# Optimization experiments

Measured on AMD Instinct MI355X. Metric: run time of the kernel, lower is better.

## Reference

```python
import jax, jax.numpy as jnp
import numpy as np

B, P = 8, 1000          # batch_size, num_prots
N = B * P               # total PPI nodes
E = 512000              # edges (avg degree 64)
F_HPO = 1024            # HPO feature dim (num_features)
F_MOLP = 8192           # protein molecular feature dim (hardcoded)
F_MOLD = 1024           # drug molecular feature dim (hardcoded)
D = 200
EPS = 1e-8              # torch CosineSimilarity default eps


def leaky(x):
    return jax.nn.leaky_relu(x, 0.2)


def gcn_improved(x, W, b, src, dst):
    # PyG GCNConv(improved=True): A_hat = A + 2*I, symmetrically normalized.
    h = x @ W                                                   # [N,200]
    deg = jnp.zeros((x.shape[0],), x.dtype).at[dst].add(1.0) + 2.0
    dinv = jax.lax.rsqrt(deg)
    norm = dinv[src] * dinv[dst]                                # [E]
    out = jnp.zeros_like(h).at[dst].add(norm[:, None] * h[src])  # gather->scale->scatter
    out = out + (2.0 * dinv * dinv)[:, None] * h                # self loops with weight 2
    return out + b


def setup_inputs() -> dict:
    key = jax.random.key(0)
    ks = jax.random.split(key, 30)
    def W(i, shape):
        return jax.random.normal(ks[i], shape, jnp.float32) * (1.0 / float(np.sqrt(shape[0])))
    def bvec(i, n):
        return jax.random.normal(ks[i], (n,), jnp.float32) * 0.01
    return {
        # forward inputs
        'PPI_x': jax.random.normal(ks[0], (N, F_HPO), jnp.float32),
        'protein_mol_feature': jax.random.normal(ks[1], (N, F_MOLP), jnp.float32),
        'drug_feature': jax.random.normal(ks[2], (B, F_HPO), jnp.float32),
        'drug_mol_feature': jax.random.normal(ks[3], (B, F_MOLD), jnp.float32),
        'edge_index': jax.random.randint(ks[4], (2, E), 0, N, dtype=jnp.int32),
        # frozen HPO model heads (assumed Linear -> 200)
        'hpo_drug_W': W(5, (F_HPO, D)), 'hpo_drug_b': bvec(6, D),
        'hpo_prot_W': W(7, (F_HPO, D)), 'hpo_prot_b': bvec(8, D),
        # mol_protein_model: 8192 -> 256 -> 200
        'mp_W1': W(9, (F_MOLP, 256)), 'mp_b1': bvec(10, 256),
        'mp_W2': W(11, (256, D)), 'mp_b2': bvec(12, D),
        # mol_drug_model: 1024 -> 256 -> 200
        'md_W1': W(13, (F_MOLD, 256)), 'md_b1': bvec(14, 256),
        'md_W2': W(15, (256, D)), 'md_b2': bvec(16, D),
        # fusion linears
        'pl1_W': W(17, (2 * D, D)), 'pl1_b': bvec(18, D),
        'dl1_W': W(19, (2 * D, D)), 'dl1_b': bvec(20, D),
        'dl2_W': W(21, (D, D)), 'dl2_b': bvec(22, D),
        # GCN layers
        'g1_W': W(23, (D, D)), 'g1_b': bvec(24, D),
        'g2_W': W(25, (D, D)), 'g2_b': bvec(26, D),
    }


def reference(PPI_x, protein_mol_feature, drug_feature, drug_mol_feature, edge_index,
              hpo_drug_W, hpo_drug_b, hpo_prot_W, hpo_prot_b,
              mp_W1, mp_b1, mp_W2, mp_b2, md_W1, md_b1, md_W2, md_b2,
              pl1_W, pl1_b, dl1_W, dl1_b, dl2_W, dl2_b,
              g1_W, g1_b, g2_W, g2_b):
    src, dst = edge_index[0], edge_index[1]
    # protein branch (dropout is identity in eval)
    px = PPI_x @ hpo_prot_W + hpo_prot_b                                 # [N,200]
    pm = leaky(protein_mol_feature @ mp_W1 + mp_b1) @ mp_W2 + mp_b2      # [N,200]
    px = leaky(jnp.concatenate([px, pm], axis=1))                        # [N,400]
    px = px @ pl1_W + pl1_b                                              # [N,200]
    # drug branch
    df = drug_feature @ hpo_drug_W + hpo_drug_b                          # [B,200]
    dm = leaky(drug_mol_feature @ md_W1 + md_b1) @ md_W2 + md_b2         # [B,200]
    d = leaky(jnp.concatenate([dm, df], axis=1))                         # [B,400]
    d = leaky(d @ dl1_W + dl1_b)                                         # [B,200]
    d = d @ dl2_W + dl2_b                                                # [B,200]
    d = jnp.repeat(d, P, axis=0)                                         # [B*P,200]
    # two stacked GCN layers (no nonlinearity between, as in source)
    px = gcn_improved(px, g1_W, g1_b, src, dst)
    px = gcn_improved(px, g2_W, g2_b, src, dst)
    # per-row cosine similarity (torch.nn.CosineSimilarity(dim=1))
    num = jnp.sum(d * px, axis=1)
    den = jnp.maximum(jnp.linalg.norm(d, axis=1), EPS) * jnp.maximum(jnp.linalg.norm(px, axis=1), EPS)
    sim = num / den
    return jax.nn.sigmoid(sim.reshape(B, P))
```

## Files before the change

### kernel.cpp

```cpp
#include <hip/hip_runtime.h>
#include <cstdint>
#include <cstddef>

typedef uint16_t u16;
typedef __bf16 bf16x8 __attribute__((ext_vector_type(8)));
typedef short  s16x8  __attribute__((ext_vector_type(8)));
typedef float  f32x4  __attribute__((ext_vector_type(4)));

__device__ __forceinline__ u16 f2b(float f) {
    union { float f; uint32_t u; } v; v.f = f;
    uint32_t u = v.u;
    uint32_t r = (u + 0x7FFFu + ((u >> 16) & 1u)) >> 16;
    return (u16)r;
}
__device__ __forceinline__ float b2f(u16 h) {
    union { uint32_t u; float f; } v; v.u = ((uint32_t)h) << 16;
    return v.f;
}
__device__ __forceinline__ float leakyf(float x) { return x > 0.f ? x : 0.2f * x; }
__device__ __forceinline__ void unp4(uint2 u, float& f0, float& f1, float& f2, float& f3) {
    union { uint32_t u; float f; } t;
    t.u = u.x << 16;          f0 = t.f;
    t.u = u.x & 0xffff0000u;  f1 = t.f;
    t.u = u.y << 16;          f2 = t.f;
    t.u = u.y & 0xffff0000u;  f3 = t.f;
}

static constexpr int NN = 8000;
static constexpr int EE = 512000;
static constexpr int BB = 8;

#define GLOAD_LDS16(gp, lp)                                                              \
    __builtin_amdgcn_global_load_lds((const __attribute__((address_space(1))) void*)(gp), \
                                     (__attribute__((address_space(3))) void*)(lp), 16, 0, 0)

__global__ void conv_wT(const float* __restrict__ W, int Wn, int rows, int rowOff,
                        u16* __restrict__ Bt, int Kpad, int kOff, int kSpan) {
    __shared__ u16 tile[64][65];
    const int kb = blockIdx.x * 64, nb = blockIdx.y * 64;
    const int tid = threadIdx.x;
    const int ln = tid & 63, lw = tid >> 6;
    #pragma unroll
    for (int r = 0; r < 16; r++) {
        int kk = kb + lw * 16 + r;
        int n  = nb + ln;
        float v = (kk < rows && n < Wn) ? W[(size_t)(rowOff + kk) * Wn + n] : 0.f;
        tile[ln][lw * 16 + r] = f2b(v);
    }
    __syncthreads();
    #pragma unroll
    for (int r = 0; r < 16; r++) {
        int nl = lw * 16 + r;
        int kk = kb + ln;
        if (kk < kSpan) Bt[(size_t)(nb + nl) * Kpad + kOff + kk] = tile[nl][ln];
    }
}

__global__ void conv_wT5(const float* W_mp2, const float* W_pl1, const float* W_g1, const float* W_g2,
                         u16* Btmp2, u16* Btpl1, u16* Btg1, u16* Btg2) {
    __shared__ u16 tile[64][65];
    const float* W; int Wn, rows, rowOff; u16* Bt; int Kpad, kOff, kSpan;
    switch (blockIdx.z) {
        case 0: W = W_mp2; Wn = 200; rows = 256; rowOff = 0;   Bt = Btmp2; Kpad = 256; kOff = 0;   kSpan = 256; break;
        case 1: W = W_pl1; Wn = 200; rows = 200; rowOff = 0;   Bt = Btpl1; Kpad = 512; kOff = 0;   kSpan = 256; break;
        case 2: W = W_pl1; Wn = 200; rows = 200; rowOff = 200; Bt = Btpl1; Kpad = 512; kOff = 256; kSpan = 256; break;
        case 3: W = W_g1;  Wn = 200; rows = 200; rowOff = 0;   Bt = Btg1;  Kpad = 256; kOff = 0;   kSpan = 256; break;
        default:W = W_g2;  Wn = 200; rows = 200; rowOff = 0;   Bt = Btg2;  Kpad = 256; kOff = 0;   kSpan = 256; break;
    }
    const int kb = blockIdx.x * 64, nb = blockIdx.y * 64;
    const int tid = threadIdx.x;
    const int ln = tid & 63, lw = tid >> 6;
    #pragma unroll
    for (int r = 0; r < 16; r++) {
        int kk = kb + lw * 16 + r;
        int n  = nb + ln;
        float v = (kk < rows && n < Wn) ? W[(size_t)(rowOff + kk) * Wn + n] : 0.f;
        tile[ln][lw * 16 + r] = f2b(v);
    }
    __syncthreads();
    #pragma unroll
    for (int r = 0; r < 16; r++) {
        int nl = lw * 16 + r;
        int kk = kb + ln;
        if (kk < kSpan) Bt[(size_t)(nb + nl) * Kpad + kOff + kk] = tile[nl][ln];
    }
}

__global__ void padvec5(const float* p0, int n0, float* d0,
                        const float* p1, int n1, float* d1,
                        const float* p2, int n2, float* d2,
                        const float* p3, int n3, float* d3,
                        const float* p4, int n4, float* d4) {
    const float* p; int n; float* d;
    switch (blockIdx.x) {
        case 0: p = p0; n = n0; d = d0; break;
        case 1: p = p1; n = n1; d = d1; break;
        case 2: p = p2; n = n2; d = d2; break;
        case 3: p = p3; n = n3; d = d3; break;
        default: p = p4; n = n4; d = d4; break;
    }
    int i = threadIdx.x;
    d[i] = (p != nullptr && i < n) ? p[i] : 0.f;
}

__global__ void zero_i32(int* __restrict__ p, int n) {
    int i = blockIdx.x * 256 + threadIdx.x;
    if (i < n) p[i] = 0;
}

__global__ __launch_bounds__(256) void gemm_kernel(
    const void* __restrict__ Ap, int a_is_f32, int lda,
    const u16* __restrict__ Bt, int K, int kLen,
    const float* __restrict__ bias,
    void* __restrict__ Cp, int cmode, int ldc, int do_leaky, size_t partStride) {
    __shared__ u16 As[2][32][72];
    __shared__ u16 Bs[2][16384];
    const int tid  = threadIdx.x;
    const int m0   = blockIdx.x * 32;
    const int kStart = blockIdx.y * kLen;
    const int wave = tid >> 6, lane = tid & 63;
    const int q = lane >> 4, r = lane & 15;
    const int wn = wave * 64;
    const int arow = tid & 31, akoff = (tid >> 5) * 8;
    const int nIter = kLen >> 6;

    f32x4 acc[2][4];
    #pragma unroll
    for (int i = 0; i < 2; i++)
        #pragma unroll
        for (int j = 0; j < 4; j++) acc[i][j] = (f32x4){0, 0, 0, 0};

    auto stageB = [&](int buf, int k0) {
        #pragma unroll
        for (int c = 0; c < 8; ++c) {
            const int idx16 = c * 256 + tid;
            const int row   = idx16 >> 3;
            const int gs    = (idx16 & 7) ^ (row & 7);
            const u16* src  = Bt + (size_t)row * K + k0 + gs * 8;
            u16* dst = &Bs[buf][0] + c * 2048 + wave * 512;
            GLOAD_LDS16(src, dst);
        }
    };
    float4 fa0, fa1; uint4 ua;
    auto loadA = [&](int k0) {
        if (a_is_f32) {
            const float* A = (const float*)Ap + (size_t)(m0 + arow) * lda + k0 + akoff;
            fa0 = *(const float4*)A;
            fa1 = *(const float4*)(A + 4);
        } else {
            const u16* A = (const u16*)Ap + (size_t)(m0 + arow) * lda + k0 + akoff;
            ua = *(const uint4*)A;
        }
    };
    auto writeA = [&](int buf) {
        uint4 w;
        if (a_is_f32) {
            u16 h[8];
            h[0] = f2b(fa0.x); h[1] = f2b(fa0.y); h[2] = f2b(fa0.z); h[3] = f2b(fa0.w);
            h[4] = f2b(fa1.x); h[5] = f2b(fa1.y); h[6] = f2b(fa1.z); h[7] = f2b(fa1.w);
            w = *(uint4*)h;
        } else w = ua;
        *(uint4*)(&As[buf][arow][akoff]) = w;
    };

    loadA(kStart);
    stageB(0, kStart);
    writeA(0);
    __syncthreads();

    int cur = 0;
    for (int t = 0; t < nIter; ++t) {
        const int nb = cur ^ 1;
        const bool hasNext = (t + 1 < nIter);
        if (hasNext) {
            const int k1 = kStart + (t + 1) * 64;
            loadA(k1);
            stageB(nb, k1);
        }
        const char* BsC = (const char*)&Bs[cur][0];
        #pragma unroll
        for (int ks = 0; ks < 2; ks++) {
            const int kb = ks * 32 + q * 8;
            s16x8 a0 = *(const s16x8*)(&As[cur][r][kb]);
            s16x8 a1 = *(const s16x8*)(&As[cur][16 + r][kb]);
            const int swz  = ((ks << 2) + q) ^ (r & 7);
            const int boff = ((wn + r) << 7) + (swz << 4);
            s16x8 b0 = *(const s16x8*)(BsC + boff);
            s16x8 b1 = *(const s16x8*)(BsC + boff + 2048);
            s16x8 b2 = *(const s16x8*)(BsC + boff + 4096);
            s16x8 b3 = *(const s16x8*)(BsC + boff + 6144);
            acc[0][0] = __builtin_amdgcn_mfma_f32_16x16x32_bf16(__builtin_bit_cast(bf16x8, a0), __builtin_bit_cast(bf16x8, b0), acc[0][0], 0, 0, 0);
            acc[0][1] = __builtin_amdgcn_mfma_f32_16x16x32_bf16(__builtin_bit_cast(bf16x8, a0), __builtin_bit_cast(bf16x8, b1), acc[0][1], 0, 0, 0);
            acc[0][2] = __builtin_amdgcn_mfma_f32_16x16x32_bf16(__builtin_bit_cast(bf16x8, a0), __builtin_bit_cast(bf16x8, b2), acc[0][2], 0, 0, 0);
            acc[0][3] = __builtin_amdgcn_mfma_f32_16x16x32_bf16(__builtin_bit_cast(bf16x8, a0), __builtin_bit_cast(bf16x8, b3), acc[0][3], 0, 0, 0);
            acc[1][0] = __builtin_amdgcn_mfma_f32_16x16x32_bf16(__builtin_bit_cast(bf16x8, a1), __builtin_bit_cast(bf16x8, b0), acc[1][0], 0, 0, 0);
            acc[1][1] = __builtin_amdgcn_mfma_f32_16x16x32_bf16(__builtin_bit_cast(bf16x8, a1), __builtin_bit_cast(bf16x8, b1), acc[1][1], 0, 0, 0);
            acc[1][2] = __builtin_amdgcn_mfma_f32_16x16x32_bf16(__builtin_bit_cast(bf16x8, a1), __builtin_bit_cast(bf16x8, b2), acc[1][2], 0, 0, 0);
            acc[1][3] = __builtin_amdgcn_mfma_f32_16x16x32_bf16(__builtin_bit_cast(bf16x8, a1), __builtin_bit_cast(bf16x8, b3), acc[1][3], 0, 0, 0);
        }
        if (hasNext) writeA(nb);
        __syncthreads();
        cur = nb;
    }

    #pragma unroll
    for (int ti = 0; ti < 2; ti++)
        #pragma unroll
        for (int tj = 0; tj < 4; tj++)
            #pragma unroll
            for (int reg = 0; reg < 4; reg++) {
                int gr = m0 + ti * 16 + q * 4 + reg;
                int gc = wn + tj * 16 + r;
                float v = acc[ti][tj][reg];
                if (cmode == 2) {
                    ((float*)Cp)[blockIdx.y * partStride + (size_t)gr * 256 + gc] = v;
                } else {
                    v += bias[gc];
                    if (do_leaky) v = leakyf(v);
                    if (cmode == 1) ((u16*)Cp)[(size_t)gr * ldc + gc] = f2b(v);
                    else            ((float*)Cp)[(size_t)gr * ldc + gc] = v;
                }
            }
}

__global__ void reduce_k(const float* __restrict__ part, size_t partStride, int S,
                         const float* __restrict__ bias, void* __restrict__ out,
                         int out_bf16, int ldc, int do_leaky) {
    int i = blockIdx.x * 256 + threadIdx.x;
    float v = 0.f;
    for (int s = 0; s < S; s++) v += part[s * partStride + i];
    int col = i & 255, row = i >> 8;
    v += bias[col];
    if (do_leaky) v = leakyf(v);
    if (out_bf16) ((u16*)out)[(size_t)row * ldc + col] = f2b(v);
    else          ((float*)out)[(size_t)row * ldc + col] = v;
}

__global__ void count_kernel(const int* __restrict__ dst, int* __restrict__ cnt) {
    int e = blockIdx.x * 256 + threadIdx.x;
    if (e < EE) atomicAdd(&cnt[dst[e]], 1);
}
__global__ void scan_kernel(const int* __restrict__ cnt, int* __restrict__ row_start,
                            int* __restrict__ cursor, float* __restrict__ dinv) {
    __shared__ int part[1024];
    const int tid = threadIdx.x;
    int local[8];
    int s = 0;
    const int base = tid * 8;
    #pragma unroll
    for (int j = 0; j < 8; j++) { int idx = base + j; int v = (idx < NN) ? cnt[idx] : 0; local[j] = s; s += v; }
    part[tid] = s;
    __syncthreads();
    for (int off = 1; off < 1024; off <<= 1) {
        int v = (tid >= off) ? part[tid - off] : 0;
        __syncthreads();
        part[tid] += v;
        __syncthreads();
    }
    const int excl = (tid == 0) ? 0 : part[tid - 1];
    #pragma unroll
    for (int j = 0; j < 8; j++) {
        int idx = base + j;
        if (idx < NN) {
            int v = excl + local[j];
            row_start[idx] = v; cursor[idx] = v;
            dinv[idx] = rsqrtf((float)cnt[idx] + 2.0f);
        }
    }
    if (tid == 1023) row_start[NN] = part[1023];
}
__global__ void fill_kernel(const int* __restrict__ src, const int* __restrict__ dst,
                            int* __restrict__ cursor, const float* __restrict__ dinv,
                            int* __restrict__ csr_src, float* __restrict__ csr_w) {
    int e = blockIdx.x * 256 + threadIdx.x;
    if (e < EE) {
        int s = src[e], d = dst[e];
        int pos = atomicAdd(&cursor[d], 1);
        csr_src[pos] = s;
        csr_w[pos]   = dinv[s] * dinv[d];
    }
}

__global__ __launch_bounds__(256) void agg_kernel(
    const u16* __restrict__ h, const float* __restrict__ dinv,
    const int* __restrict__ row_start, const int* __restrict__ csr_src,
    const float* __restrict__ csr_w, const float* __restrict__ bias,
    u16* __restrict__ out_bf16, const float* __restrict__ dhat,
    float* __restrict__ out_sig) {
    const int wave = threadIdx.x >> 6, lane = threadIdx.x & 63;
    const int node = blockIdx.x * 4 + wave;
    const int start = row_start[node], end = row_start[node + 1];
    const float di = dinv[node];

    float a0, a1, a2, a3;
    {
        uint2 hv = *(const uint2*)(h + (size_t)node * 256 + lane * 4);
        float f0, f1, f2, f3; unp4(hv, f0, f1, f2, f3);
        float sl = 2.f * di * di;
        a0 = sl * f0; a1 = sl * f1; a2 = sl * f2; a3 = sl * f3;
    }

    for (int p = start; p < end; p += 64) {
        const int n = min(64, end - p);
        int   mySrc = 0;
        float myW   = 0.f;
        if (lane < n) { mySrc = csr_src[p + lane]; myW = csr_w[p + lane]; }
        int j0 = 0;
        for (; j0 + 8 <= n; j0 += 8) {
            int sj[8]; float wj[8]; uint2 rj[8];
            #pragma unroll
            for (int j = 0; j < 8; j++) { sj[j] = __shfl(mySrc, j0 + j); wj[j] = __shfl(myW, j0 + j); }
            #pragma unroll
            for (int j = 0; j < 8; j++) rj[j] = *(const uint2*)(h + (size_t)sj[j] * 256 + lane * 4);
            #pragma unroll
            for (int j = 0; j < 8; j++) {
                float f0, f1, f2, f3; unp4(rj[j], f0, f1, f2, f3);
                a0 += wj[j] * f0; a1 += wj[j] * f1; a2 += wj[j] * f2; a3 += wj[j] * f3;
            }
        }
        for (; j0 < n; j0++) {
            int s = __shfl(mySrc, j0);
            float w = __shfl(myW, j0);
            uint2 rv = *(const uint2*)(h + (size_t)s * 256 + lane * 4);
            float f0, f1, f2, f3; unp4(rv, f0, f1, f2, f3);
            a0 += w * f0; a1 += w * f1; a2 += w * f2; a3 += w * f3;
        }
    }

    if (out_bf16 != nullptr) {
        uint2 o = {0u, 0u};
        if (lane < 50) {
            float4 bv = *(const float4*)(bias + lane * 4);
            u16 h0 = f2b(a0 + bv.x), h1 = f2b(a1 + bv.y), h2 = f2b(a2 + bv.z), h3 = f2b(a3 + bv.w);
            o.x = (uint32_t)h0 | ((uint32_t)h1 << 16);
            o.y = (uint32_t)h2 | ((uint32_t)h3 << 16);
        }
        *(uint2*)(out_bf16 + (size_t)node * 256 + lane * 4) = o;
    } else {
        float dot = 0.f, nn2 = 0.f;
        if (lane < 50) {
            float4 bv = *(const float4*)(bias + lane * 4);
            float4 dv = *(const float4*)(dhat + (node / 1000) * 200 + lane * 4);
            float v0 = a0 + bv.x, v1 = a1 + bv.y, v2 = a2 + bv.z, v3 = a3 + bv.w;
            dot = v0 * dv.x + v1 * dv.y + v2 * dv.z + v3 * dv.w;
            nn2 = v0 * v0 + v1 * v1 + v2 * v2 + v3 * v3;
        }
        #pragma unroll
        for (int off = 32; off; off >>= 1) {
            dot += __shfl_xor(dot, off, 64);
            nn2 += __shfl_xor(nn2, off, 64);
        }
        if (lane == 0) {
            float sim = dot / fmaxf(sqrtf(nn2), 1e-8f);
            out_sig[node] = 1.f / (1.f + expf(-sim));
        }
    }
}

__global__ void drug_kernel(const float* __restrict__ drugF, const float* __restrict__ drugM,
                            const float* __restrict__ hW, const float* __restrict__ hb,
                            const float* __restrict__ m1W, const float* __restrict__ m1b,
                            const float* __restrict__ m2W, const float* __restrict__ m2b,
                            const float* __restrict__ l1W, const float* __restrict__ l1b,
                            const float* __restrict__ l2W, const float* __restrict__ l2b,
                            float* __restrict__ dhat) {
    const int b = blockIdx.x, tid = threadIdx.x;
    __shared__ float sF[1024], sM[1024], sT[256], s400[400], s200[200], sred[256];
    for (int k = tid; k < 1024; k += 256) { sF[k] = drugF[b * 1024 + k]; sM[k] = drugM[b * 1024 + k]; }
    __syncthreads();
    {
        float acc = m1b[tid];
        for (int k = 0; k < 1024; k++) acc += sM[k] * m1W[k * 256 + tid];
        sT[tid] = leakyf(acc);
    }
    float dfv = 0.f;
    if (tid < 200) {
        dfv = hb[tid];
        for (int k = 0; k < 1024; k++) dfv += sF[k] * hW[k * 200 + tid];
    }
    __syncthreads();
    if (tid < 200) {
        float acc = m2b[tid];
        for (int k = 0; k < 256; k++) acc += sT[k] * m2W[k * 200 + tid];
        s400[tid]       = leakyf(acc);
        s400[200 + tid] = leakyf(dfv);
    }
    __syncthreads();
    if (tid < 200) {
        float acc = l1b[tid];
        for (int k = 0; k < 400; k++) acc += s400[k] * l1W[k * 200 + tid];
        s200[tid] = leakyf(acc);
    }
    __syncthreads();
    float dv = 0.f;
    if (tid < 200) {
        dv = l2b[tid];
        for (int k = 0; k < 200; k++) dv += s200[k] * l2W[k * 200 + tid];
    }
    sred[tid] = (tid < 200) ? dv * dv : 0.f;
    __syncthreads();
    for (int off = 128; off; off >>= 1) {
        if (tid < off) sred[tid] += sred[tid + off];
        __syncthreads();
    }
    float nrm = fmaxf(sqrtf(sred[0]), 1e-8f);
    if (tid < 200) dhat[b * 200 + tid] = dv / nrm;
}

extern "C" void kernel_launch(void* const* d_in, const int* in_sizes, int n_in,
                              void* d_out, int out_size, void* d_ws, size_t ws_size,
                              hipStream_t stream) {
    const float* PPI_x = (const float*)d_in[0];
    const float* PMF   = (const float*)d_in[1];
    const float* drugF = (const float*)d_in[2];
    const float* drugM = (const float*)d_in[3];
    const int*   eidx  = (const int*)d_in[4];
    const float* hpo_drug_W = (const float*)d_in[5];
    const float* hpo_drug_b = (const float*)d_in[6];
    const float* hpo_prot_W = (const float*)d_in[7];
    const float* hpo_prot_b = (const float*)d_in[8];
    const float* mp_W1 = (const float*)d_in[9];
    const float* mp_b1 = (const float*)d_in[10];
    const float* mp_W2 = (const float*)d_in[11];
    const float* mp_b2 = (const float*)d_in[12];
    const float* md_W1 = (const float*)d_in[13];
    const float* md_b1 = (const float*)d_in[14];
    const float* md_W2 = (const float*)d_in[15];
    const float* md_b2 = (const float*)d_in[16];
    const float* pl1_W = (const float*)d_in[17];
    const float* pl1_b = (const float*)d_in[18];
    const float* dl1_W = (const float*)d_in[19];
    const float* dl1_b = (const float*)d_in[20];
    const float* dl2_W = (const float*)d_in[21];
    const float* dl2_b = (const float*)d_in[22];
    const float* g1_W  = (const float*)d_in[23];
    const float* g1_b  = (const float*)d_in[24];
    const float* g2_W  = (const float*)d_in[25];
    const float* g2_b  = (const float*)d_in[26];

    char* wsp = (char*)d_ws;
    size_t off = 0;
    auto alloc = [&](size_t bytes) -> void* {
        size_t o = (off + 255) & ~(size_t)255;
        off = o + bytes;
        return (void*)(wsp + o);
    };

    u16* cb    = (u16*)alloc((size_t)NN * 512 * 2);
    u16* t1    = (u16*)alloc((size_t)NN * 256 * 2);
    u16* px2   = (u16*)alloc((size_t)NN * 256 * 2);
    u16* hbuf  = (u16*)alloc((size_t)NN * 256 * 2);
    float* part = (float*)alloc((size_t)2 * NN * 256 * 4);
    u16* Btmp1 = (u16*)alloc((size_t)256 * 8192 * 2);
    u16* Bthpo = (u16*)alloc((size_t)256 * 1024 * 2);
    u16* Btmp2 = (u16*)alloc((size_t)256 * 256 * 2);
    u16* Btpl1 = (u16*)alloc((size_t)256 * 512 * 2);
    u16* Btg1  = (u16*)alloc((size_t)256 * 256 * 2);
    u16* Btg2  = (u16*)alloc((size_t)256 * 256 * 2);
    float* bias_hpo = (float*)alloc(256 * 4);
    float* bias_m1  = (float*)alloc(256 * 4);
    float* bias_m2  = (float*)alloc(256 * 4);
    float* bias_pl  = (float*)alloc(256 * 4);
    float* zero256  = (float*)alloc(256 * 4);
    float* dhat     = (float*)alloc((size_t)BB * 200 * 4);
    int*   deg      = (int*)alloc((size_t)NN * 4);
    float* dinv     = (float*)alloc((size_t)NN * 4);
    int*   row_st   = (int*)alloc((size_t)(NN + 4) * 4);
    int*   cursor   = (int*)alloc((size_t)NN * 4);
    int*   csr_src  = (int*)alloc((size_t)EE * 4);
    float* csr_w    = (float*)alloc((size_t)EE * 4);

    u16* y1 = t1;
    const size_t PSTRIDE = (size_t)NN * 256;

    const int* e_src = eidx;
    const int* e_dst = eidx + EE;

    conv_wT<<<dim3(16, 4),  256, 0, stream>>>(hpo_prot_W, 200, 1024, 0, Bthpo, 1024, 0, 1024);
    conv_wT<<<dim3(128, 4), 256, 0, stream>>>(mp_W1,      256, 8192, 0, Btmp1, 8192, 0, 8192);
    conv_wT5<<<dim3(4, 4, 5), 256, 0, stream>>>(mp_W2, pl1_W, g1_W, g2_W, Btmp2, Btpl1, Btg1, Btg2);
    padvec5<<<5, 256, 0, stream>>>(hpo_prot_b, 200, bias_hpo,
                                   mp_b1,      256, bias_m1,
                                   mp_b2,      200, bias_m2,
                                   pl1_b,      200, bias_pl,
                                   nullptr,    0,   zero256);

    drug_kernel<<<BB, 256, 0, stream>>>(drugF, drugM, hpo_drug_W, hpo_drug_b,
                                        md_W1, md_b1, md_W2, md_b2,
                                        dl1_W, dl1_b, dl2_W, dl2_b, dhat);

    const int MB = NN / 32;
    const int RG = (NN * 256) / 256;

    gemm_kernel<<<dim3(MB, 1), 256, 0, stream>>>(PPI_x, 1, 1024, Bthpo, 1024, 1024, bias_hpo, cb, 1, 512, 1, 0);
    gemm_kernel<<<dim3(MB, 2), 256, 0, stream>>>(PMF, 1, 8192, Btmp1, 8192, 4096, zero256, part, 2, 256, 0, PSTRIDE);
    reduce_k<<<RG, 256, 0, stream>>>(part, PSTRIDE, 2, bias_m1, t1, 1, 256, 1);
    gemm_kernel<<<dim3(MB, 1), 256, 0, stream>>>(t1, 0, 256, Btmp2, 256, 256, bias_m2, cb + 256, 1, 512, 1, 0);
    gemm_kernel<<<dim3(MB, 1), 256, 0, stream>>>(cb, 0, 512, Btpl1, 512, 512, bias_pl, px2, 1, 256, 0, 0);

    zero_i32<<<(NN + 255) / 256, 256, 0, stream>>>(deg, NN);
    count_kernel<<<EE / 256, 256, 0, stream>>>(e_dst, deg);
    scan_kernel<<<1, 1024, 0, stream>>>(deg, row_st, cursor, dinv);
    fill_kernel<<<EE / 256, 256, 0, stream>>>(e_src, e_dst, cursor, dinv, csr_src, csr_w);

    gemm_kernel<<<dim3(MB, 1), 256, 0, stream>>>(px2, 0, 256, Btg1, 256, 256, zero256, hbuf, 1, 256, 0, 0);
    agg_kernel<<<NN / 4, 256, 0, stream>>>(hbuf, dinv, row_st, csr_src, csr_w, g1_b, y1, nullptr, nullptr);
    gemm_kernel<<<dim3(MB, 1), 256, 0, stream>>>(y1, 0, 256, Btg2, 256, 256, zero256, hbuf, 1, 256, 0, 0);
    agg_kernel<<<NN / 4, 256, 0, stream>>>(hbuf, dinv, row_st, csr_src, csr_w, g2_b, nullptr, dhat, (float*)d_out);
}
```

Before: 906.6 us.

## Deepen GEMM A-prefetch with manual waitcnt pipelining and split-K the HPO GEMM

The GEMM main loop is unrolled by two, with two register sets for A so the A loads for step t+2 are issued while step t computes. The generic __syncthreads is replaced by explicit s_waitcnt vmcnt counts and raw s_barrier/sched_barrier, which lets global loads stay in flight across the barrier. The HPO protein GEMM is also split along K into two partial blocks followed by a reduce, doubling its grid. The hand-tuned vmcnt values depend on the exact number of outstanding loads, so a wrong count could race, and the added reduce kernel costs an extra pass over memory.

```diff
diff --git a/kernel.cpp b/kernel.cpp
--- a/kernel.cpp
+++ b/kernel.cpp
@@ -122,7 +122,7 @@
     const int q = lane >> 4, r = lane & 15;
     const int wn = wave * 64;
     const int arow = tid & 31, akoff = (tid >> 5) * 8;
-    const int nIter = kLen >> 6;
+    const int n = kLen >> 6;
 
     f32x4 acc[2][4];
     #pragma unroll
@@ -141,67 +141,114 @@
             GLOAD_LDS16(src, dst);
         }
     };
-    float4 fa0, fa1; uint4 ua;
-    auto loadA = [&](int k0) {
+
+    float4 f0a, f1a, f0b, f1b; uint4 uA, uB;
+    auto issueA_set0 = [&](int k0) {
         if (a_is_f32) {
             const float* A = (const float*)Ap + (size_t)(m0 + arow) * lda + k0 + akoff;
-            fa0 = *(const float4*)A;
-            fa1 = *(const float4*)(A + 4);
+            f0a = *(const float4*)A; f1a = *(const float4*)(A + 4);
         } else {
             const u16* A = (const u16*)Ap + (size_t)(m0 + arow) * lda + k0 + akoff;
-            ua = *(const uint4*)A;
+            uA = *(const uint4*)A;
         }
     };
-    auto writeA = [&](int buf) {
+    auto issueA_set1 = [&](int k0) {
+        if (a_is_f32) {
+            const float* A = (const float*)Ap + (size_t)(m0 + arow) * lda + k0 + akoff;
+            f0b = *(const float4*)A; f1b = *(const float4*)(A + 4);
+        } else {
+            const u16* A = (const u16*)Ap + (size_t)(m0 + arow) * lda + k0 + akoff;
+            uB = *(const uint4*)A;
+        }
+    };
+    auto writeA_set0 = [&](int buf) {
         uint4 w;
         if (a_is_f32) {
             u16 h[8];
-            h[0] = f2b(fa0.x); h[1] = f2b(fa0.y); h[2] = f2b(fa0.z); h[3] = f2b(fa0.w);
-            h[4] = f2b(fa1.x); h[5] = f2b(fa1.y); h[6] = f2b(fa1.z); h[7] = f2b(fa1.w);
+            h[0] = f2b(f0a.x); h[1] = f2b(f0a.y); h[2] = f2b(f0a.z); h[3] = f2b(f0a.w);
+            h[4] = f2b(f1a.x); h[5] = f2b(f1a.y); h[6] = f2b(f1a.z); h[7] = f2b(f1a.w);
             w = *(uint4*)h;
-        } else w = ua;
+        } else w = uA;
         *(uint4*)(&As[buf][arow][akoff]) = w;
     };
-
-    loadA(kStart);
+    auto writeA_set1 = [&](int buf) {
+        uint4 w;
+        if (a_is_f32) {
+            u16 h[8];
+            h[0] = f2b(f0b.x); h[1] = f2b(f0b.y); h[2] = f2b(f0b.z); h[3] = f2b(f0b.w);
+            h[4] = f2b(f1b.x); h[5] = f2b(f1b.y); h[6] = f2b(f1b.z); h[7] = f2b(f1b.w);
+            w = *(uint4*)h;
+        } else w = uB;
+        *(uint4*)(&As[buf][arow][akoff]) = w;
+    };
+
+#define GEMM_WAIT(hasA, hasB)                                                                   \
+    do {                                                                                        \
+        if (hasA) {                                                                             \
+            if (a_is_f32) asm volatile("s_waitcnt vmcnt(10) lgkmcnt(0)" ::: "memory");           \
+            else          asm volatile("s_waitcnt vmcnt(9) lgkmcnt(0)"  ::: "memory");           \
+        } else if (hasB)  asm volatile("s_waitcnt vmcnt(8) lgkmcnt(0)"  ::: "memory");           \
+        else              asm volatile("s_waitcnt vmcnt(0) lgkmcnt(0)"  ::: "memory");           \
+    } while (0)
+
+#define MFMA_PHASE(CUR)                                                                         \
+    do {                                                                                        \
+        const char* BsC = (const char*)&Bs[CUR][0];                                             \
+        _Pragma("unroll")                                                                       \
+        for (int ks = 0; ks < 2; ks++) {                                                        \
+            const int kb = ks * 32 + q * 8;                                                     \
+            s16x8 a0 = *(const s16x8*)(&As[CUR][r][kb]);                                        \
+            s16x8 a1 = *(const s16x8*)(&As[CUR][16 + r][kb]);                                   \
+            const int swz  = ((ks << 2) + q) ^ (r & 7);                                         \
+            const int boff = ((wn + r) << 7) + (swz << 4);                                      \
+            s16x8 b0 = *(const s16x8*)(BsC + boff);                                             \
+            s16x8 b1 = *(const s16x8*)(BsC + boff + 2048);                                      \
+            s16x8 b2 = *(const s16x8*)(BsC + boff + 4096);                                      \
+            s16x8 b3 = *(const s16x8*)(BsC + boff + 6144);                                      \
+            acc[0][0] = __builtin_amdgcn_mfma_f32_16x16x32_bf16(__builtin_bit_cast(bf16x8, a0), __builtin_bit_cast(bf16x8, b0), acc[0][0], 0, 0, 0); \
+            acc[0][1] = __builtin_amdgcn_mfma_f32_16x16x32_bf16(__builtin_bit_cast(bf16x8, a0), __builtin_bit_cast(bf16x8, b1), acc[0][1], 0, 0, 0); \
+            acc[0][2] = __builtin_amdgcn_mfma_f32_16x16x32_bf16(__builtin_bit_cast(bf16x8, a0), __builtin_bit_cast(bf16x8, b2), acc[0][2], 0, 0, 0); \
+            acc[0][3] = __builtin_amdgcn_mfma_f32_16x16x32_bf16(__builtin_bit_cast(bf16x8, a0), __builtin_bit_cast(bf16x8, b3), acc[0][3], 0, 0, 0); \
+            acc[1][0] = __builtin_amdgcn_mfma_f32_16x16x32_bf16(__builtin_bit_cast(bf16x8, a1), __builtin_bit_cast(bf16x8, b0), acc[1][0], 0, 0, 0); \
+            acc[1][1] = __builtin_amdgcn_mfma_f32_16x16x32_bf16(__builtin_bit_cast(bf16x8, a1), __builtin_bit_cast(bf16x8, b1), acc[1][1], 0, 0, 0); \
+            acc[1][2] = __builtin_amdgcn_mfma_f32_16x16x32_bf16(__builtin_bit_cast(bf16x8, a1), __builtin_bit_cast(bf16x8, b2), acc[1][2], 0, 0, 0); \
+            acc[1][3] = __builtin_amdgcn_mfma_f32_16x16x32_bf16(__builtin_bit_cast(bf16x8, a1), __builtin_bit_cast(bf16x8, b3), acc[1][3], 0, 0, 0); \
+        }                                                                                       \
+    } while (0)
+
+    issueA_set0(kStart);
     stageB(0, kStart);
-    writeA(0);
-    __syncthreads();
-
-    int cur = 0;
-    for (int t = 0; t < nIter; ++t) {
-        const int nb = cur ^ 1;
-        const bool hasNext = (t + 1 < nIter);
-        if (hasNext) {
-            const int k1 = kStart + (t + 1) * 64;
-            loadA(k1);
-            stageB(nb, k1);
-        }
-        const char* BsC = (const char*)&Bs[cur][0];
-        #pragma unroll
-        for (int ks = 0; ks < 2; ks++) {
-            const int kb = ks * 32 + q * 8;
-            s16x8 a0 = *(const s16x8*)(&As[cur][r][kb]);
-            s16x8 a1 = *(const s16x8*)(&As[cur][16 + r][kb]);
-            const int swz  = ((ks << 2) + q) ^ (r & 7);
-            const int boff = ((wn + r) << 7) + (swz << 4);
-            s16x8 b0 = *(const s16x8*)(BsC + boff);
-            s16x8 b1 = *(const s16x8*)(BsC + boff + 2048);
-            s16x8 b2 = *(const s16x8*)(BsC + boff + 4096);
-            s16x8 b3 = *(const s16x8*)(BsC + boff + 6144);
-            acc[0][0] = __builtin_amdgcn_mfma_f32_16x16x32_bf16(__builtin_bit_cast(bf16x8, a0), __builtin_bit_cast(bf16x8, b0), acc[0][0], 0, 0, 0);
-            acc[0][1] = __builtin_amdgcn_mfma_f32_16x16x32_bf16(__builtin_bit_cast(bf16x8, a0), __builtin_bit_cast(bf16x8, b1), acc[0][1], 0, 0, 0);
-            acc[0][2] = __builtin_amdgcn_mfma_f32_16x16x32_bf16(__builtin_bit_cast(bf16x8, a0), __builtin_bit_cast(bf16x8, b2), acc[0][2], 0, 0, 0);
-            acc[0][3] = __builtin_amdgcn_mfma_f32_16x16x32_bf16(__builtin_bit_cast(bf16x8, a0), __builtin_bit_cast(bf16x8, b3), acc[0][3], 0, 0, 0);
-            acc[1][0] = __builtin_amdgcn_mfma_f32_16x16x32_bf16(__builtin_bit_cast(bf16x8, a1), __builtin_bit_cast(bf16x8, b0), acc[1][0], 0, 0, 0);
-            acc[1][1] = __builtin_amdgcn_mfma_f32_16x16x32_bf16(__builtin_bit_cast(bf16x8, a1), __builtin_bit_cast(bf16x8, b1), acc[1][1], 0, 0, 0);
-            acc[1][2] = __builtin_amdgcn_mfma_f32_16x16x32_bf16(__builtin_bit_cast(bf16x8, a1), __builtin_bit_cast(bf16x8, b2), acc[1][2], 0, 0, 0);
-            acc[1][3] = __builtin_amdgcn_mfma_f32_16x16x32_bf16(__builtin_bit_cast(bf16x8, a1), __builtin_bit_cast(bf16x8, b3), acc[1][3], 0, 0, 0);
-        }
-        if (hasNext) writeA(nb);
-        __syncthreads();
-        cur = nb;
-    }
+    if (n > 1) issueA_set1(kStart + 64);
+    writeA_set0(0);
+
+    for (int t = 0; t < n; t += 2) {
+        {
+            const bool hasA = t + 2 < n, hasB = t + 1 < n;
+            if (hasA) issueA_set0(kStart + (t + 2) * 64);
+            if (hasB) stageB(1, kStart + (t + 1) * 64);
+            GEMM_WAIT(hasA, hasB);
+            __builtin_amdgcn_s_barrier();
+            __builtin_amdgcn_sched_barrier(0);
+            MFMA_PHASE(0);
+            if (hasB) writeA_set1(1);
+            asm volatile("s_waitcnt lgkmcnt(0)" ::: "memory");
+            __builtin_amdgcn_s_barrier();
+        }
+        {
+            const bool hasA = t + 3 < n, hasB = t + 2 < n;
+            if (hasA) issueA_set1(kStart + (t + 3) * 64);
+            if (hasB) stageB(0, kStart + (t + 2) * 64);
+            GEMM_WAIT(hasA, hasB);
+            __builtin_amdgcn_s_barrier();
+            __builtin_amdgcn_sched_barrier(0);
+            MFMA_PHASE(1);
+            if (hasB) writeA_set0(0);
+            asm volatile("s_waitcnt lgkmcnt(0)" ::: "memory");
+            __builtin_amdgcn_s_barrier();
+        }
+    }
+#undef GEMM_WAIT
+#undef MFMA_PHASE
 
     #pragma unroll
     for (int ti = 0; ti < 2; ti++)
@@ -492,7 +539,8 @@
     const int MB = NN / 32;
     const int RG = (NN * 256) / 256;
 
-    gemm_kernel<<<dim3(MB, 1), 256, 0, stream>>>(PPI_x, 1, 1024, Bthpo, 1024, 1024, bias_hpo, cb, 1, 512, 1, 0);
+    gemm_kernel<<<dim3(MB, 2), 256, 0, stream>>>(PPI_x, 1, 1024, Bthpo, 1024, 512, zero256, part, 2, 256, 0, PSTRIDE);
+    reduce_k<<<RG, 256, 0, stream>>>(part, PSTRIDE, 2, bias_hpo, cb, 1, 512, 1);
     gemm_kernel<<<dim3(MB, 2), 256, 0, stream>>>(PMF, 1, 8192, Btmp1, 8192, 4096, zero256, part, 2, 256, 0, PSTRIDE);
     reduce_k<<<RG, 256, 0, stream>>>(part, PSTRIDE, 2, bias_m1, t1, 1, 256, 1);
     gemm_kernel<<<dim3(MB, 1), 256, 0, stream>>>(t1, 0, 256, Btmp2, 256, 256, bias_m2, cb + 256, 1, 512, 1, 0);
```

Result: no change. 899.5 us (-0.8%).
